# Kernel tuning notes

Measured on AMD Instinct MI355X. Metric: run time of the kernel, lower is better.

## Reference

```python
import jax, jax.numpy as jnp
import numpy as np

NEG_SLOPE = 0.01  # torch leaky_relu default

N_NODES = 100000
N_EDGES = 1600000
D = 64
N_BBOX = 4096


def setup_inputs() -> dict:
    key = jax.random.key(0)
    ks = jax.random.split(key, 9)
    x = jax.random.normal(ks[0], (N_NODES, D), dtype=jnp.float32)
    edge_index = jax.random.randint(ks[1], (2, N_EDGES), 0, N_NODES, dtype=jnp.int64)
    bbox = jax.random.randint(ks[2], (N_BBOX,), 0, N_NODES, dtype=jnp.int64)
    s = 1.0 / np.sqrt(D)
    W1_rel = jax.random.normal(ks[3], (D, D), dtype=jnp.float32) * s
    b1 = jax.random.normal(ks[4], (D,), dtype=jnp.float32) * s
    W1_root = jax.random.normal(ks[5], (D, D), dtype=jnp.float32) * s
    W2_rel = jax.random.normal(ks[6], (D, D), dtype=jnp.float32) * s
    b2 = jax.random.normal(ks[7], (D,), dtype=jnp.float32) * s
    W2_root = jax.random.normal(ks[8], (D, D), dtype=jnp.float32) * s
    return {"x": x, "edge_index": edge_index, "bbox": bbox,
            "W1_rel": W1_rel, "b1": b1, "W1_root": W1_root,
            "W2_rel": W2_rel, "b2": b2, "W2_root": W2_root}


def graph_conv(x, src, dst, W_rel, b, W_root):
    # PyG GraphConv: out_i = W_rel @ (sum_{j in N(i)} x_j) + b + W_root @ x_i
    msg = x[src]                                        # [E, D] gather
    agg = jax.ops.segment_sum(msg, dst, num_segments=x.shape[0])  # [N, D] scatter-add
    return agg @ W_rel + b + x @ W_root


def reference(x, edge_index, bbox, W1_rel, b1, W1_root, W2_rel, b2, W2_root):
    src, dst = edge_index[0], edge_index[1]
    h = graph_conv(x, src, dst, W1_rel, b1, W1_root)
    h = jax.nn.leaky_relu(h, NEG_SLOPE)
    # dropout is identity at inference (training=False)
    h = graph_conv(h, src, dst, W2_rel, b2, W2_root)
    h = jax.nn.leaky_relu(h, NEG_SLOPE)
    return h[bbox]
```

## Files before the change

kernel.cpp:

```cpp
#include <hip/hip_runtime.h>

#define N_NODES 100000
#define N_EDGES 1600000
#define D 64
#define N_BBOX 4096
#define CAP 64
#define NBITW 3136
#define NTILE1 (N_NODES / 16)
#define NTILE2 (N_BBOX / 16)

typedef short bf16x8 __attribute__((ext_vector_type(8)));
typedef float f32x4 __attribute__((ext_vector_type(4)));

__device__ __forceinline__ int bperm(int srclane, int v) {
  return __builtin_amdgcn_ds_bpermute(srclane << 2, v);
}
__device__ __forceinline__ float lrelu(float v) {
  return fmaxf(v, 0.01f * v);
}
__device__ __forceinline__ bool testbit(const unsigned* bits, int i) {
  return (bits[i >> 5] >> (i & 31)) & 1u;
}
__device__ __forceinline__ short f2bf(float f) {
  unsigned u = __float_as_uint(f);
  u += 0x7FFFu + ((u >> 16) & 1u);
  return (short)(u >> 16);
}

__global__ __launch_bounds__(256) void mark_bbox_kernel(
    const int* __restrict__ bbox, unsigned* __restrict__ is_bbox_bits,
    unsigned* __restrict__ needed_bits) {
  const int t = blockIdx.x * 256 + threadIdx.x;
  const int n = bbox[t];
  const unsigned m = 1u << (n & 31);
  atomicOr(&is_bbox_bits[n >> 5], m);
  atomicOr(&needed_bits[n >> 5], m);
}

__global__ __launch_bounds__(256) void prep_kernel(const float4* __restrict__ x4,
                                                   bf16x8* __restrict__ xb,
                                                   const int* __restrict__ src,
                                                   const int* __restrict__ dst,
                                                   const unsigned* __restrict__ is_bbox_bits,
                                                   unsigned* __restrict__ needed_bits,
                                                   int* __restrict__ cnt,
                                                   const float* __restrict__ W1rel,
                                                   const float* __restrict__ W1root,
                                                   const float* __restrict__ W2rel,
                                                   const float* __restrict__ W2root,
                                                   short* __restrict__ wf) {
  const int i = blockIdx.x * 256 + threadIdx.x;
  if (i < N_NODES) cnt[i] = 0;
  if (i < N_NODES * 8) {
    const float4 a = x4[i * 2], b = x4[i * 2 + 1];
    bf16x8 r;
    r[0] = f2bf(a.x); r[1] = f2bf(a.y); r[2] = f2bf(a.z); r[3] = f2bf(a.w);
    r[4] = f2bf(b.x); r[5] = f2bf(b.y); r[6] = f2bf(b.z); r[7] = f2bf(b.w);
    xb[i] = r;
  } else {
    const int t = i - N_NODES * 8;
    if (t < 4 * 4096) {
      const int layer = t >> 13;
      const int r = t & 8191;
      const int m = r >> 12;
      const int e = r & 4095;
      const int kh = e >> 11, quad = (e >> 9) & 3;
      const int col = (e >> 3) & 63, ii = e & 7;
      const int k = kh * 32 + quad * 8 + ii;
      const float* W = layer ? (m ? W2root : W2rel) : (m ? W1root : W1rel);
      wf[t] = f2bf(W[k * 64 + col]);
    } else {
      const int e = t - 4 * 4096;
      if (e < N_EDGES) {
        if (testbit(is_bbox_bits, dst[e]))
          atomicOr(&needed_bits[src[e] >> 5], 1u << (src[e] & 31));
      }
    }
  }
}

__global__ __launch_bounds__(256) void scatter_kernel(
    const int* __restrict__ src, const int* __restrict__ dst,
    const unsigned* __restrict__ needed_bits, int* __restrict__ cnt,
    int* __restrict__ slots) {
  const int e = blockIdx.x * 256 + threadIdx.x;
  const int d = dst[e];
  if (!testbit(needed_bits, d)) return;
  const int s = src[e];
  const int pos = atomicAdd(&cnt[d], 1);
  if (pos < CAP) slots[(size_t)d * CAP + pos] = s;
}

__device__ __forceinline__ void gather_rows(const uint4* __restrict__ rows,
                                            const int* __restrict__ slots,
                                            int node, int n, int lane,
                                            float accf[8]) {
  const int g = lane >> 3, c = lane & 7;
  const int myslot = (lane < n) ? slots[(size_t)node * CAP + lane] : 0;
#pragma unroll
  for (int i = 0; i < 8; i++) accf[i] = 0.f;
  for (int e0 = 0; e0 < n; e0 += 32) {
    const int rem = n - e0;
    int idx[4], s[4];
    uint4 v[4];
#pragma unroll
    for (int u = 0; u < 4; u++)
      if (u * 8 < rem) {
        idx[u] = e0 + u * 8 + g;
        s[u] = bperm(idx[u], myslot);
      }
#pragma unroll
    for (int u = 0; u < 4; u++)
      if (u * 8 < rem) {
        v[u] = make_uint4(0u, 0u, 0u, 0u);
        if (idx[u] < n) v[u] = rows[(size_t)s[u] * 8 + c];
      }
#pragma unroll
    for (int u = 0; u < 4; u++)
      if (u * 8 < rem) {
        accf[0] += __uint_as_float(v[u].x << 16);
        accf[1] += __uint_as_float(v[u].x & 0xFFFF0000u);
        accf[2] += __uint_as_float(v[u].y << 16);
        accf[3] += __uint_as_float(v[u].y & 0xFFFF0000u);
        accf[4] += __uint_as_float(v[u].z << 16);
        accf[5] += __uint_as_float(v[u].z & 0xFFFF0000u);
        accf[6] += __uint_as_float(v[u].w << 16);
        accf[7] += __uint_as_float(v[u].w & 0xFFFF0000u);
      }
  }
#pragma unroll
  for (int off = 8; off < 64; off <<= 1)
#pragma unroll
    for (int i = 0; i < 8; i++) accf[i] += __shfl_xor(accf[i], off);
}

__global__ __launch_bounds__(256) void gd1_kernel(
    const uint4* __restrict__ xb4, const short* __restrict__ xb,
    const unsigned* __restrict__ needed_bits, const int* __restrict__ cnt,
    const int* __restrict__ slots, const short* __restrict__ wf1,
    const float* __restrict__ b1, short* __restrict__ hb) {
  __shared__ __align__(16) short aggt[16][72];
  const int t = threadIdx.x;
  const int lane = t & 63;
  const int wid = t >> 6;
  const int cn = lane & 15, quad = lane >> 4;
  const int col = wid * 16 + cn;
  const int node0 = blockIdx.x * 16;

  const bf16x8* wfv = (const bf16x8*)wf1;
  bf16x8 brel[2], broot[2];
#pragma unroll
  for (int kh = 0; kh < 2; kh++) {
    brel[kh] = wfv[(kh * 4 + quad) * 64 + col];
    broot[kh] = wfv[((2 + kh) * 4 + quad) * 64 + col];
  }
  const float bj = b1[col];

#pragma unroll
  for (int r4 = 0; r4 < 4; r4++) {
    const int row = wid * 4 + r4;
    const int node = node0 + row;
    int n = cnt[node];
    n = (n > CAP) ? CAP : n;
    if (n == 0) {
      if (lane < 8) {
        bf16x8 z = {0, 0, 0, 0, 0, 0, 0, 0};
        *(bf16x8*)(&aggt[row][lane * 8]) = z;
      }
      continue;
    }
    float accf[8];
    gather_rows(xb4, slots, node, n, lane, accf);
    if (lane < 8) {
      bf16x8 r;
#pragma unroll
      for (int i = 0; i < 8; i++) r[i] = f2bf(accf[i]);
      *(bf16x8*)(&aggt[row][lane * 8]) = r;
    }
  }
  __syncthreads();

  const int mrow = node0 + cn;
  const bool ndrow = testbit(needed_bits, mrow);
  f32x4 acc = {};
#pragma unroll
  for (int kh = 0; kh < 2; kh++) {
    const bf16x8 a_agg = *(const bf16x8*)(&aggt[cn][kh * 32 + quad * 8]);
    bf16x8 a_x = {0, 0, 0, 0, 0, 0, 0, 0};
    if (ndrow)
      a_x = *(const bf16x8*)(xb + (size_t)mrow * D + kh * 32 + quad * 8);
    acc = __builtin_amdgcn_mfma_f32_16x16x32_bf16(a_agg, brel[kh], acc, 0, 0, 0);
    acc = __builtin_amdgcn_mfma_f32_16x16x32_bf16(a_x, broot[kh], acc, 0, 0, 0);
  }
#pragma unroll
  for (int r = 0; r < 4; r++) {
    const int row = quad * 4 + r;
    if (testbit(needed_bits, node0 + row))
      hb[(size_t)(node0 + row) * D + col] = f2bf(lrelu(acc[r] + bj));
  }
}

__global__ __launch_bounds__(256) void gd2_kernel(
    const uint4* __restrict__ hb4, const short* __restrict__ hb,
    const int* __restrict__ cnt, const int* __restrict__ slots,
    const int* __restrict__ bbox, const short* __restrict__ wf2,
    const float* __restrict__ b2, float* __restrict__ out) {
  __shared__ __align__(16) short aggt[16][72];
  __shared__ int nodes_s[16];
  const int t = threadIdx.x;
  const int lane = t & 63;
  const int wid = t >> 6;
  const int cn = lane & 15, quad = lane >> 4;
  const int col = wid * 16 + cn;
  const int t0 = blockIdx.x * 16;

  if (t < 16) nodes_s[t] = bbox[t0 + t];

  const bf16x8* wfv = (const bf16x8*)wf2;
  bf16x8 brel[2], broot[2];
#pragma unroll
  for (int kh = 0; kh < 2; kh++) {
    brel[kh] = wfv[(kh * 4 + quad) * 64 + col];
    broot[kh] = wfv[((2 + kh) * 4 + quad) * 64 + col];
  }
  const float bj = b2[col];
  __syncthreads();

#pragma unroll
  for (int r4 = 0; r4 < 4; r4++) {
    const int row = wid * 4 + r4;
    const int node = nodes_s[row];
    int n = cnt[node];
    n = (n > CAP) ? CAP : n;
    if (n == 0) {
      if (lane < 8) {
        bf16x8 z = {0, 0, 0, 0, 0, 0, 0, 0};
        *(bf16x8*)(&aggt[row][lane * 8]) = z;
      }
      continue;
    }
    float accf[8];
    gather_rows(hb4, slots, node, n, lane, accf);
    if (lane < 8) {
      bf16x8 r;
#pragma unroll
      for (int i = 0; i < 8; i++) r[i] = f2bf(accf[i]);
      *(bf16x8*)(&aggt[row][lane * 8]) = r;
    }
  }
  __syncthreads();

  const int rnode = nodes_s[cn];
  f32x4 acc = {};
#pragma unroll
  for (int kh = 0; kh < 2; kh++) {
    const bf16x8 a_agg = *(const bf16x8*)(&aggt[cn][kh * 32 + quad * 8]);
    const bf16x8 a_h = *(const bf16x8*)(hb + (size_t)rnode * D + kh * 32 + quad * 8);
    acc = __builtin_amdgcn_mfma_f32_16x16x32_bf16(a_agg, brel[kh], acc, 0, 0, 0);
    acc = __builtin_amdgcn_mfma_f32_16x16x32_bf16(a_h, broot[kh], acc, 0, 0, 0);
  }
#pragma unroll
  for (int r = 0; r < 4; r++) {
    const int row = quad * 4 + r;
    out[(size_t)(t0 + row) * D + col] = lrelu(acc[r] + bj);
  }
}


extern "C" void kernel_launch(void* const* d_in, const int* in_sizes, int n_in,
                              void* d_out, int out_size, void* d_ws, size_t ws_size,
                              hipStream_t stream) {
  const float* x = (const float*)d_in[0];
  const int* ei = (const int*)d_in[1];
  const int* src = ei;
  const int* dst = ei + N_EDGES;
  const int* bbox = (const int*)d_in[2];
  const float* W1rel = (const float*)d_in[3];
  const float* b1 = (const float*)d_in[4];
  const float* W1root = (const float*)d_in[5];
  const float* W2rel = (const float*)d_in[6];
  const float* b2 = (const float*)d_in[7];
  const float* W2root = (const float*)d_in[8];
  float* out = (float*)d_out;

  char* ws = (char*)d_ws;
  size_t off = 0;
  auto alloc = [&](size_t bytes) -> char* {
    char* p = ws + off;
    off = (off + bytes + 511) & ~(size_t)511;
    return p;
  };
  unsigned* is_bbox_bits = (unsigned*)alloc(NBITW * sizeof(unsigned));
  unsigned* needed_bits = (unsigned*)alloc(NBITW * sizeof(unsigned));
  char* zero_end = ws + off;
  int* cnt = (int*)alloc(N_NODES * sizeof(int));
  int* slots = (int*)alloc((size_t)N_NODES * CAP * sizeof(int));
  short* xb = (short*)alloc((size_t)N_NODES * D * sizeof(short));
  short* hb = (short*)alloc((size_t)N_NODES * D * sizeof(short));
  short* wf = (short*)alloc((size_t)4 * 4096 * sizeof(short));

  hipMemsetAsync(is_bbox_bits, 0, (size_t)(zero_end - (char*)is_bbox_bits), stream);
  mark_bbox_kernel<<<N_BBOX / 256, 256, 0, stream>>>(bbox, is_bbox_bits,
                                                     needed_bits);
  prep_kernel<<<(N_NODES * 8 + 4 * 4096 + N_EDGES + 255) / 256, 256, 0, stream>>>(
      (const float4*)x, (bf16x8*)xb, src, dst, is_bbox_bits, needed_bits, cnt,
      W1rel, W1root, W2rel, W2root, wf);
  scatter_kernel<<<N_EDGES / 256, 256, 0, stream>>>(src, dst, needed_bits, cnt,
                                                    slots);
  gd1_kernel<<<NTILE1, 256, 0, stream>>>((const uint4*)xb, xb, needed_bits, cnt,
                                         slots, wf, b1, hb);
  gd2_kernel<<<NTILE2, 256, 0, stream>>>((const uint4*)hb, hb, cnt, slots, bbox,
                                         wf + 8192, b2, out);
}
```

Before: 193.2 us.

## Merge edge marking and CSR scatter into slice-partitioned kernel, fold bbox marking into prep

Removes the separate bbox-marking kernel by folding it into prep. The needed-source marking pass and the slot scatter become one kernel. Each block handles one edge stripe and one of eight node-ID slices, so atomics on cnt, slots and needed_bits stay within a smaller address range and get better L2 locality. The scatter now fills slots for every destination rather than only needed ones, and the first aggregation kernel checks needed_bits before reading cnt. Each edge is read eight times (once per slice), and both src and dst are loaded for every edge.

```diff
diff --git a/kernel.cpp b/kernel.cpp
--- a/kernel.cpp
+++ b/kernel.cpp
@@ -6,6 +6,9 @@
 #define N_BBOX 4096
 #define CAP 64
 #define NBITW 3136
+#define SLICE 12500
+#define NSTRIPE 256
+#define EPB (N_EDGES / NSTRIPE)
 #define NTILE1 (N_NODES / 16)
 #define NTILE2 (N_BBOX / 16)
 
@@ -27,30 +30,17 @@
   return (short)(u >> 16);
 }
 
-__global__ __launch_bounds__(256) void mark_bbox_kernel(
-    const int* __restrict__ bbox, unsigned* __restrict__ is_bbox_bits,
-    unsigned* __restrict__ needed_bits) {
-  const int t = blockIdx.x * 256 + threadIdx.x;
-  const int n = bbox[t];
-  const unsigned m = 1u << (n & 31);
-  atomicOr(&is_bbox_bits[n >> 5], m);
-  atomicOr(&needed_bits[n >> 5], m);
-}
-
 __global__ __launch_bounds__(256) void prep_kernel(const float4* __restrict__ x4,
                                                    bf16x8* __restrict__ xb,
-                                                   const int* __restrict__ src,
-                                                   const int* __restrict__ dst,
-                                                   const unsigned* __restrict__ is_bbox_bits,
+                                                   const int* __restrict__ bbox,
+                                                   unsigned* __restrict__ is_bbox_bits,
                                                    unsigned* __restrict__ needed_bits,
-                                                   int* __restrict__ cnt,
                                                    const float* __restrict__ W1rel,
                                                    const float* __restrict__ W1root,
                                                    const float* __restrict__ W2rel,
                                                    const float* __restrict__ W2root,
                                                    short* __restrict__ wf) {
   const int i = blockIdx.x * 256 + threadIdx.x;
-  if (i < N_NODES) cnt[i] = 0;
   if (i < N_NODES * 8) {
     const float4 a = x4[i * 2], b = x4[i * 2 + 1];
     bf16x8 r;
@@ -59,36 +49,49 @@
     xb[i] = r;
   } else {
     const int t = i - N_NODES * 8;
-    if (t < 4 * 4096) {
-      const int layer = t >> 13;
-      const int r = t & 8191;
+    if (t < N_BBOX) {
+      const int n = bbox[t];
+      const unsigned m = 1u << (n & 31);
+      atomicOr(&is_bbox_bits[n >> 5], m);
+      atomicOr(&needed_bits[n >> 5], m);
+    } else if (t < N_BBOX + 4 * 4096) {
+      const int t2 = t - N_BBOX;
+      const int layer = t2 >> 13;
+      const int r = t2 & 8191;
       const int m = r >> 12;
       const int e = r & 4095;
       const int kh = e >> 11, quad = (e >> 9) & 3;
       const int col = (e >> 3) & 63, ii = e & 7;
       const int k = kh * 32 + quad * 8 + ii;
       const float* W = layer ? (m ? W2root : W2rel) : (m ? W1root : W1rel);
-      wf[t] = f2bf(W[k * 64 + col]);
-    } else {
-      const int e = t - 4 * 4096;
-      if (e < N_EDGES) {
-        if (testbit(is_bbox_bits, dst[e]))
-          atomicOr(&needed_bits[src[e] >> 5], 1u << (src[e] & 31));
-      }
-    }
-  }
-}
-
-__global__ __launch_bounds__(256) void scatter_kernel(
+      wf[t2] = f2bf(W[k * 64 + col]);
+    }
+  }
+}
+
+__global__ __launch_bounds__(256) void scatterM_kernel(
     const int* __restrict__ src, const int* __restrict__ dst,
-    const unsigned* __restrict__ needed_bits, int* __restrict__ cnt,
+    const unsigned* __restrict__ is_bbox_bits,
+    unsigned* __restrict__ needed_bits, int* __restrict__ cnt,
     int* __restrict__ slots) {
-  const int e = blockIdx.x * 256 + threadIdx.x;
-  const int d = dst[e];
-  if (!testbit(needed_bits, d)) return;
-  const int s = src[e];
-  const int pos = atomicAdd(&cnt[d], 1);
-  if (pos < CAP) slots[(size_t)d * CAP + pos] = s;
+  const int sl = blockIdx.x & 7;
+  const int stripe = blockIdx.x >> 3;
+  const int lo = sl * SLICE;
+  const int hi = lo + SLICE;
+  const int e0 = stripe * EPB;
+  for (int i = threadIdx.x; i < EPB; i += 256) {
+    const int e = e0 + i;
+    const int d = dst[e];
+    const int s = src[e];
+    if (d >= lo && d < hi) {
+      const int pos = atomicAdd(&cnt[d], 1);
+      if (pos < CAP) slots[(size_t)d * CAP + pos] = s;
+    }
+    if (s >= lo && s < hi) {
+      if (testbit(is_bbox_bits, d))
+        atomicOr(&needed_bits[s >> 5], 1u << (s & 31));
+    }
+  }
 }
 
 __device__ __forceinline__ void gather_rows(const uint4* __restrict__ rows,
@@ -160,8 +163,11 @@
   for (int r4 = 0; r4 < 4; r4++) {
     const int row = wid * 4 + r4;
     const int node = node0 + row;
-    int n = cnt[node];
-    n = (n > CAP) ? CAP : n;
+    int n = 0;
+    if (testbit(needed_bits, node)) {
+      n = cnt[node];
+      n = (n > CAP) ? CAP : n;
+    }
     if (n == 0) {
       if (lane < 8) {
         bf16x8 z = {0, 0, 0, 0, 0, 0, 0, 0};
@@ -292,21 +298,19 @@
   };
   unsigned* is_bbox_bits = (unsigned*)alloc(NBITW * sizeof(unsigned));
   unsigned* needed_bits = (unsigned*)alloc(NBITW * sizeof(unsigned));
+  int* cnt = (int*)alloc(N_NODES * sizeof(int));
   char* zero_end = ws + off;
-  int* cnt = (int*)alloc(N_NODES * sizeof(int));
   int* slots = (int*)alloc((size_t)N_NODES * CAP * sizeof(int));
   short* xb = (short*)alloc((size_t)N_NODES * D * sizeof(short));
   short* hb = (short*)alloc((size_t)N_NODES * D * sizeof(short));
   short* wf = (short*)alloc((size_t)4 * 4096 * sizeof(short));
 
   hipMemsetAsync(is_bbox_bits, 0, (size_t)(zero_end - (char*)is_bbox_bits), stream);
-  mark_bbox_kernel<<<N_BBOX / 256, 256, 0, stream>>>(bbox, is_bbox_bits,
-                                                     needed_bits);
-  prep_kernel<<<(N_NODES * 8 + 4 * 4096 + N_EDGES + 255) / 256, 256, 0, stream>>>(
-      (const float4*)x, (bf16x8*)xb, src, dst, is_bbox_bits, needed_bits, cnt,
+  prep_kernel<<<(N_NODES * 8 + N_BBOX + 4 * 4096 + 255) / 256, 256, 0, stream>>>(
+      (const float4*)x, (bf16x8*)xb, bbox, is_bbox_bits, needed_bits,
       W1rel, W1root, W2rel, W2root, wf);
-  scatter_kernel<<<N_EDGES / 256, 256, 0, stream>>>(src, dst, needed_bits, cnt,
-                                                    slots);
+  scatterM_kernel<<<8 * NSTRIPE, 256, 0, stream>>>(src, dst, is_bbox_bits,
+                                                   needed_bits, cnt, slots);
   gd1_kernel<<<NTILE1, 256, 0, stream>>>((const uint4*)xb, xb, needed_bits, cnt,
                                          slots, wf, b1, hb);
   gd2_kernel<<<NTILE2, 256, 0, stream>>>((const uint4*)hb, hb, cnt, slots, bbox,
```

Result: slower. 216.6 us (+12.1%).
